# Kernel tuning notes

Measured on AMD Instinct MI355X. Metric: run time of the kernel, lower is better.

The kernel has to match this reference:

```python
import jax, jax.numpy as jnp
import numpy as np

KH, KW = 3, 3
T_MIN, T_MAX = 0.0, 1.0  # default layer params (set_params never called)


def setup_inputs() -> dict:
    key = jax.random.key(0)
    k1, k2, k3 = jax.random.split(key, 3)
    # spike times in [0, 1]
    tj = jax.random.uniform(k1, (16, 258, 258), dtype=jnp.float32)
    # (filters, 1, kh, kw), scaled so outputs are not all clamped at t_max
    kernel = jax.random.normal(k2, (128, 1, KH, KW), dtype=jnp.float32) * 0.05
    D_i = jax.random.normal(k3, (9, 128), dtype=jnp.float32) * 0.01
    return {"tj": tj, "kernel": kernel, "D_i": D_i}


def reference(tj, kernel, D_i):
    # tj: [B, S, S]; valid padding, default branch (BN buffer == 0).
    B, S, _ = tj.shape
    Hv = S - KH + 1  # image_valid_size
    Fc = kernel.shape[0]
    # torch: W = kernel.view(-1, filters) -> row-major reinterpretation of (F,1,kh,kw) as (9, F)
    W = kernel.reshape(KH * KW, Fc)
    # 3x3 patches per (batch-as-channel) map, kernel taps in row-major (ki, kj) order
    patches = jnp.stack(
        [tj[:, i:i + Hv, j:j + Hv] for i in range(KH) for j in range(KW)],
        axis=-1,
    )  # [B, Hv, Hv, 9]
    # torch unfold layout: row index = patch_l * B + channel_c
    X = jnp.transpose(patches, (1, 2, 0, 3)).reshape(-1, KH * KW)  # [Hv*Hv*B, 9]
    threshold = (T_MAX - T_MIN) - D_i[0]  # (F,)
    ti = (X - T_MIN) @ W + threshold + T_MIN  # [N, F]
    ti = jnp.where(ti < T_MAX, ti, T_MAX)  # clamp late spikes to t_max
    return ti.reshape(-1, Hv, Hv, Fc)  # matches torch .view(-1, Hv, Hv, F)
```

## Files before the change

### kernel.cpp

```cpp
#include <hip/hip_runtime.h>


#define B_N   16
#define S_N   258
#define HV_N  256
#define F_N   128

typedef float v4f __attribute__((ext_vector_type(4)));

__global__ __launch_bounds__(256, 6) void spiking_conv2d_kernel(
    const float* __restrict__ tj, const float* __restrict__ kern,
    const float* __restrict__ Di, float* __restrict__ out, int num_groups) {
  const int fq   = threadIdx.x & 31;
  const int nsub = threadIdx.x >> 5;

  float4 w[9];
#pragma unroll
  for (int t = 0; t < 9; ++t)
    w[t] = reinterpret_cast<const float4*>(kern)[t * (F_N / 4) + fq];
  const float4 d = reinterpret_cast<const float4*>(Di)[fq];
  const float4 thr = make_float4(1.0f - d.x, 1.0f - d.y, 1.0f - d.z, 1.0f - d.w);

  for (int g = blockIdx.x; g < num_groups; g += gridDim.x) {
    const int n   = g * 8 + nsub;
    const int b   = n & (B_N - 1);
    const int pix = n >> 4;
    const int j   = pix & (HV_N - 1);
    const int i   = pix >> 8;

    const float* base = tj + (b * S_N + i) * S_N + j;
    float x[9];
#pragma unroll
    for (int ki = 0; ki < 3; ++ki)
#pragma unroll
      for (int kj = 0; kj < 3; ++kj)
        x[ki * 3 + kj] = base[ki * S_N + kj];

    float4 acc = thr;
#pragma unroll
    for (int t = 0; t < 9; ++t) {
      acc.x = fmaf(x[t], w[t].x, acc.x);
      acc.y = fmaf(x[t], w[t].y, acc.y);
      acc.z = fmaf(x[t], w[t].z, acc.z);
      acc.w = fmaf(x[t], w[t].w, acc.w);
    }
    v4f v = {fminf(acc.x, 1.0f), fminf(acc.y, 1.0f),
             fminf(acc.z, 1.0f), fminf(acc.w, 1.0f)};
    __builtin_nontemporal_store(v, reinterpret_cast<v4f*>(out) + n * (F_N / 4) + fq);
  }
}

extern "C" void kernel_launch(void* const* d_in, const int* in_sizes, int n_in,
                              void* d_out, int out_size, void* d_ws, size_t ws_size,
                              hipStream_t stream) {
  const float* tj   = (const float*)d_in[0];
  const float* kern = (const float*)d_in[1];
  const float* Di   = (const float*)d_in[2];
  float* out = (float*)d_out;

  const int num_groups = (HV_N * HV_N * B_N) / 8;
  const int grid = 8192;
  spiking_conv2d_kernel<<<grid, 256, 0, stream>>>(tj, kern, Di, out, num_groups);
}
```

Measured before the change: 575.2 us.

## Assign four-pixel row strips per wave with software-pipelined double-buffered loads

Each 64-lane wave now owns a task of four adjacent output pixels for one batch, and each lane covers two filters using float2 weights. A 3x6 input window is loaded once and reused across the four pixels. The next task's window is prefetched into a second register buffer while the current one is computed and stored. Together these cut redundant input loads and hide load latency. The costs are more registers and narrower 8-byte nontemporal stores, on a kernel that is mostly bound by output write bandwidth.

```diff
diff --git a/kernel.cpp b/kernel.cpp
--- a/kernel.cpp
+++ b/kernel.cpp
@@ -6,48 +6,81 @@
 #define HV_N  256
 #define F_N   128
 
-typedef float v4f __attribute__((ext_vector_type(4)));
+#define GRID      8192
+#define WPB       4
+#define NSTREAM   (GRID * WPB)
+#define NTASK     ((HV_N * (HV_N / 4)) * B_N)
+
+typedef float v2f __attribute__((ext_vector_type(2)));
 
 __global__ __launch_bounds__(256, 6) void spiking_conv2d_kernel(
     const float* __restrict__ tj, const float* __restrict__ kern,
-    const float* __restrict__ Di, float* __restrict__ out, int num_groups) {
-  const int fq   = threadIdx.x & 31;
-  const int nsub = threadIdx.x >> 5;
+    const float* __restrict__ Di, float* __restrict__ out) {
+  const int lane = threadIdx.x & 63;
+  const int wid  = __builtin_amdgcn_readfirstlane(threadIdx.x >> 6);
 
-  float4 w[9];
+  float2 w[9];
 #pragma unroll
   for (int t = 0; t < 9; ++t)
-    w[t] = reinterpret_cast<const float4*>(kern)[t * (F_N / 4) + fq];
-  const float4 d = reinterpret_cast<const float4*>(Di)[fq];
-  const float4 thr = make_float4(1.0f - d.x, 1.0f - d.y, 1.0f - d.z, 1.0f - d.w);
+    w[t] = reinterpret_cast<const float2*>(kern)[t * (F_N / 2) + lane];
+  const float2 d = reinterpret_cast<const float2*>(Di)[lane];
+  const float thx = 1.0f - d.x, thy = 1.0f - d.y;
 
-  for (int g = blockIdx.x; g < num_groups; g += gridDim.x) {
-    const int n   = g * 8 + nsub;
-    const int b   = n & (B_N - 1);
-    const int pix = n >> 4;
-    const int j   = pix & (HV_N - 1);
-    const int i   = pix >> 8;
+  auto load_task = [&](int t, float (&x)[18]) {
+    const int b    = t & (B_N - 1);
+    const int pblk = t >> 4;
+    const int j0   = (pblk & 63) << 2;
+    const int i    = pblk >> 6;
+    const float* s = tj + (b * S_N + i) * S_N + j0;
+#pragma unroll
+    for (int r = 0; r < 3; ++r)
+#pragma unroll
+      for (int c = 0; c < 6; ++c)
+        x[r * 6 + c] = s[r * S_N + c];
+  };
 
-    const float* base = tj + (b * S_N + i) * S_N + j;
-    float x[9];
+  auto compute_store = [&](int t, const float (&x)[18]) {
+    const int b    = t & (B_N - 1);
+    const int pblk = t >> 4;
+    const int j0   = (pblk & 63) << 2;
+    const int i    = pblk >> 6;
+    const int n0   = ((i * HV_N + j0) << 4) | b;
+    v2f* o = reinterpret_cast<v2f*>(out) + (long)n0 * (F_N / 2) + lane;
 #pragma unroll
-    for (int ki = 0; ki < 3; ++ki)
+    for (int p = 0; p < 4; ++p) {
+      float ax = thx, ay = thy;
 #pragma unroll
-      for (int kj = 0; kj < 3; ++kj)
-        x[ki * 3 + kj] = base[ki * S_N + kj];
+      for (int r = 0; r < 3; ++r)
+#pragma unroll
+        for (int c = 0; c < 3; ++c) {
+          const float xv = x[r * 6 + p + c];
+          ax = fmaf(xv, w[r * 3 + c].x, ax);
+          ay = fmaf(xv, w[r * 3 + c].y, ay);
+        }
+      v2f v = {fminf(ax, 1.0f), fminf(ay, 1.0f)};
+      __builtin_nontemporal_store(v, o + p * (16 * (F_N / 2)));
+    }
+  };
 
-    float4 acc = thr;
-#pragma unroll
-    for (int t = 0; t < 9; ++t) {
-      acc.x = fmaf(x[t], w[t].x, acc.x);
-      acc.y = fmaf(x[t], w[t].y, acc.y);
-      acc.z = fmaf(x[t], w[t].z, acc.z);
-      acc.w = fmaf(x[t], w[t].w, acc.w);
+  float xa[18], xb[18];
+  int t = blockIdx.x * WPB + wid;
+  if (t >= NTASK) return;
+  load_task(t, xa);
+#pragma unroll 1
+  for (; t + NSTREAM < NTASK; ) {
+    load_task(t + NSTREAM, xb);
+    compute_store(t, xa);
+    t += NSTREAM;
+    if (t + NSTREAM < NTASK) {
+      load_task(t + NSTREAM, xa);
+      compute_store(t, xb);
+      t += NSTREAM;
+    } else {
+      compute_store(t, xb);
+      t += NSTREAM;
     }
-    v4f v = {fminf(acc.x, 1.0f), fminf(acc.y, 1.0f),
-             fminf(acc.z, 1.0f), fminf(acc.w, 1.0f)};
-    __builtin_nontemporal_store(v, reinterpret_cast<v4f*>(out) + n * (F_N / 4) + fq);
   }
+  if (t < NTASK) compute_store(t, xa);
 }
 
 extern "C" void kernel_launch(void* const* d_in, const int* in_sizes, int n_in,
@@ -57,8 +90,5 @@
   const float* kern = (const float*)d_in[1];
   const float* Di   = (const float*)d_in[2];
   float* out = (float*)d_out;
-
-  const int num_groups = (HV_N * HV_N * B_N) / 8;
-  const int grid = 8192;
-  spiking_conv2d_kernel<<<grid, 256, 0, stream>>>(tj, kern, Di, out, num_groups);
+  spiking_conv2d_kernel<<<GRID, 256, 0, stream>>>(tj, kern, Di, out);
 }
```

Result: faster. 530.1 us (-7.8%).
